# Kernel tuning notes

Measured on AMD Instinct MI355X. Metric: run time of the kernel, lower is better.

## Reference

```python
import jax, jax.numpy as jnp
import numpy as np

N = 20000   # nodes
E = 320000  # edges
F0 = 32     # num_features
H = 8       # GAT heads
G = 64      # graphs in batch


def setup_inputs() -> dict:
    key = jax.random.key(0)
    ks = jax.random.split(key, 16)
    def p(k, shape, s=0.05):
        return jax.random.normal(k, shape, jnp.float32) * s
    d = {}
    d['x'] = jax.random.normal(ks[0], (N, F0), jnp.float32)
    d['edge_index'] = jax.random.randint(ks[1], (2, E), 0, N, dtype=jnp.int32)
    d['edge_weights'] = jax.random.uniform(ks[2], (E,), jnp.float32)
    d['batch'] = jnp.sort(jax.random.randint(ks[3], (N,), 0, G, dtype=jnp.int32))
    # GATConv(32 -> 32, heads=8)
    d['W_gat'] = p(ks[4], (F0, H * F0)); d['att_src'] = p(ks[5], (H, F0))
    d['att_dst'] = p(ks[6], (H, F0));    d['b_gat'] = jnp.zeros((H * F0,), jnp.float32)
    # residual Linear(256 -> 1024) (widened so the residual add is shape-consistent)
    d['W_res'] = p(ks[7], (H * F0, 1024)); d['b_res'] = jnp.zeros((1024,), jnp.float32)
    # GCNConv(256 -> 512) + BN1
    d['W2'] = p(ks[8], (H * F0, 512)); d['b2'] = jnp.zeros((512,), jnp.float32)
    d['g1'] = jnp.ones((512,), jnp.float32); d['be1'] = jnp.zeros((512,), jnp.float32)
    d['m1'] = jnp.zeros((512,), jnp.float32); d['v1'] = jnp.ones((512,), jnp.float32)
    # GCNConv(512 -> 1024) + BN2
    d['W3'] = p(ks[9], (512, 1024)); d['b3'] = jnp.zeros((1024,), jnp.float32)
    d['g2'] = jnp.ones((1024,), jnp.float32); d['be2'] = jnp.zeros((1024,), jnp.float32)
    d['m2'] = jnp.zeros((1024,), jnp.float32); d['v2'] = jnp.ones((1024,), jnp.float32)
    # head
    d['Wf1'] = p(ks[10], (1024, 256)); d['bf1'] = jnp.zeros((256,), jnp.float32)
    d['Wf2'] = p(ks[11], (256, 2));    d['bf2'] = jnp.zeros((2,), jnp.float32)
    return d


def _add_self_loops(edge_index, edge_weight, n):
    loop = jnp.arange(n, dtype=edge_index.dtype)
    ei = jnp.concatenate([edge_index, jnp.stack([loop, loop])], axis=1)
    ew = jnp.concatenate([edge_weight, jnp.ones((n,), edge_weight.dtype)])
    return ei, ew


def _gat(x, edge_index, W, att_src, att_dst, b, n):
    # PyG GATConv, concat=True, eval (attention dropout off). Self-loops already added.
    src, dst = edge_index[0], edge_index[1]
    h = (x @ W).reshape(n, H, -1)                    # [N,H,C]
    a_s = jnp.einsum('nhc,hc->nh', h, att_src)        # [N,H]
    a_d = jnp.einsum('nhc,hc->nh', h, att_dst)
    e = jax.nn.leaky_relu(a_s[src] + a_d[dst], 0.2)   # [E,H]
    m = jax.ops.segment_max(e, dst, num_segments=n)   # softmax over incoming edges
    ex = jnp.exp(e - m[dst])
    s = jax.ops.segment_sum(ex, dst, num_segments=n)
    alpha = ex / s[dst]
    out = jax.ops.segment_sum(h[src] * alpha[:, :, None], dst, num_segments=n)
    return out.reshape(n, -1) + b                     # [N,H*C]


def _gcn(x, edge_index, w, W, b, n):
    # PyG GCNConv with symmetric normalization; self-loops (weight 1) already added.
    src, dst = edge_index[0], edge_index[1]
    deg = jax.ops.segment_sum(w, dst, num_segments=n)
    dinv = jnp.where(deg > 0, jax.lax.rsqrt(jnp.maximum(deg, 1e-12)), 0.0)
    norm = dinv[src] * w * dinv[dst]                  # [E]
    h = x @ W                                         # transform first (cheaper)
    return jax.ops.segment_sum(h[src] * norm[:, None], dst, num_segments=n) + b


def _bn(x, g, b, m, v):
    return g * (x - m) * jax.lax.rsqrt(v + 1e-5) + b


def reference(x, edge_index, edge_weights, batch, W_gat, att_src, att_dst, b_gat,
              W_res, b_res, W2, b2, g1, be1, m1, v1, W3, b3, g2, be2, m2, v2,
              Wf1, bf1, Wf2, bf2):
    n = x.shape[0]
    ei, ew = _add_self_loops(edge_index, edge_weights, n)
    h = jax.nn.relu(_gat(x, ei, W_gat, att_src, att_dst, b_gat, n))   # [N,256]
    res = h @ W_res + b_res                                           # [N,1024]
    h = _gcn(h, ei, ew, W2, b2, n)                                    # [N,512]
    h = jax.nn.relu(_bn(h, g1, be1, m1, v1))
    h = _gcn(h, ei, ew, W3, b3, n)                                    # [N,1024]
    h = jax.nn.relu(_bn(h, g2, be2, m2, v2))
    h = h + res
    pooled = jax.ops.segment_max(h, batch, num_segments=G)            # global max pool [G,1024]
    z = jax.nn.relu(pooled @ Wf1 + bf1)                               # dropout is eval no-op
    return z @ Wf2 + bf2                                              # [G,2]
```

## Files before the change

kernel.cpp:

```cpp
#include <hip/hip_runtime.h>
#include <hip/hip_bf16.h>

#define NN 20000
#define EE 320000
#define GG 64
#define EN (EE + NN)
#define MT 157
#define SB 79

typedef float f32x4 __attribute__((ext_vector_type(4)));
typedef __bf16 bf16x4 __attribute__((ext_vector_type(4)));
typedef __bf16 bf16x8 __attribute__((ext_vector_type(8)));

__device__ __forceinline__ void gl_lds16(const void* g, void* l) {
    __builtin_amdgcn_global_load_lds((const __attribute__((address_space(1))) void*)g,
                                     (__attribute__((address_space(3))) void*)l, 16, 0, 0);
}

__global__ void sentinel_kernel(float* out, int n) {
    int i = blockIdx.x * 256 + threadIdx.x;
    if (i < n) out[i] = 12345.0f;
}

__global__ void init_kernel(int* deg_cnt, float* deg_w, int* fill, float* pooled) {
    int i = blockIdx.x * 256 + threadIdx.x;
    if (i < NN) { deg_cnt[i] = 1; deg_w[i] = 1.0f; fill[i] = 0; }
    if (i < GG * 1024) pooled[i] = -INFINITY;
}

__global__ void deg_kernel(const int* __restrict__ ei, const float* __restrict__ ew,
                           int* deg_cnt, float* deg_w) {
    int e = blockIdx.x * 256 + threadIdx.x;
    if (e >= EE) return;
    int dst = ei[EE + e];
    atomicAdd(&deg_cnt[dst], 1);
    atomicAdd(&deg_w[dst], ew[e]);
}

__global__ __launch_bounds__(256) void scan_blocks(const int* __restrict__ deg_cnt, int* __restrict__ bsum) {
    __shared__ int red[256];
    int tid = threadIdx.x, i = blockIdx.x * 256 + tid;
    red[tid] = (i < NN) ? deg_cnt[i] : 0;
    __syncthreads();
    for (int s = 128; s > 0; s >>= 1) { if (tid < s) red[tid] += red[tid + s]; __syncthreads(); }
    if (tid == 0) bsum[blockIdx.x] = red[0];
}

__global__ void scan_top(int* __restrict__ bsum, int* __restrict__ rowptr) {
    if (threadIdx.x == 0) {
        int run = 0;
        for (int i = 0; i < SB; i++) { int t = bsum[i]; bsum[i] = run; run += t; }
        rowptr[NN] = run;
    }
}

__global__ __launch_bounds__(256) void scan_write(const int* __restrict__ deg_cnt,
                                                  const int* __restrict__ bsum, int* __restrict__ rowptr) {
    __shared__ int sc[256];
    int tid = threadIdx.x, b = blockIdx.x, i = b * 256 + tid;
    int v = (i < NN) ? deg_cnt[i] : 0;
    sc[tid] = v;
    __syncthreads();
    for (int ofs = 1; ofs < 256; ofs <<= 1) {
        int t = (tid >= ofs) ? sc[tid - ofs] : 0;
        __syncthreads();
        sc[tid] += t;
        __syncthreads();
    }
    if (i < NN) rowptr[i] = bsum[b] + sc[tid] - v;
}

__global__ void fill_kernel(const int* __restrict__ ei, const float* __restrict__ ew,
                            const float* __restrict__ deg_w, const int* __restrict__ rowptr,
                            int* fill, int* __restrict__ csr_src, float* __restrict__ csr_norm) {
    int e = blockIdx.x * 256 + threadIdx.x;
    if (e >= EN) return;
    int src, dst; float w;
    if (e < EE) { src = ei[e]; dst = ei[EE + e]; w = ew[e]; }
    else        { src = dst = e - EE; w = 1.0f; }
    int pos = atomicAdd(&fill[dst], 1);
    int slot = rowptr[dst] + pos;
    csr_src[slot] = src;
    csr_norm[slot] = rsqrtf(deg_w[src]) * w * rsqrtf(deg_w[dst]);
}

__global__ __launch_bounds__(256) void convert_all(
    const float* __restrict__ W2, const float* __restrict__ W3, const float* __restrict__ Wres,
    __bf16* __restrict__ W2t, __bf16* __restrict__ W3t, __bf16* __restrict__ Wrt)
{
    __shared__ float tile[64][65];
    int b = blockIdx.x;
    const float* W; __bf16* Wt; int K, N, bx, by;
    if (b < 32)       { W = W2;   Wt = W2t; K = 256; N = 512;  int bb = b;       bx = bb & 7;  by = bb >> 3; }
    else if (b < 160) { W = W3;   Wt = W3t; K = 512; N = 1024; int bb = b - 32;  bx = bb & 15; by = bb >> 4; }
    else              { W = Wres; Wt = Wrt; K = 256; N = 1024; int bb = b - 160; bx = bb & 15; by = bb >> 4; }
    int kb = by * 64, nb = bx * 64;
    int tx = threadIdx.x & 63, ty = threadIdx.x >> 6;
#pragma unroll
    for (int i = ty; i < 64; i += 4)
        tile[i][tx] = W[(size_t)(kb + i) * N + nb + tx];
    __syncthreads();
#pragma unroll
    for (int i = ty; i < 64; i += 4)
        Wt[(size_t)(nb + i) * K + kb + tx] = (__bf16)tile[tx][i];
}


__global__ __launch_bounds__(256) void a_compute(
    const float* __restrict__ x, const float* __restrict__ W,
    const float* __restrict__ att_s, const float* __restrict__ att_d,
    float* __restrict__ a_s, float* __restrict__ a_d)
{
    __shared__ float wss[8][32], wsd[8][32];
    __shared__ float xs[32][33];
    int tid = threadIdx.x;
    {
        int h = tid >> 5, k = tid & 31;
        float s = 0.f, d = 0.f;
#pragma unroll
        for (int c = 0; c < 32; c++) {
            float wv = W[k * 256 + h * 32 + c];
            s += wv * att_s[h * 32 + c];
            d += wv * att_d[h * 32 + c];
        }
        wss[h][k] = s; wsd[h][k] = d;
    }
    __syncthreads();
    for (int n0 = blockIdx.x * 32; n0 < NN; n0 += gridDim.x * 32) {
#pragma unroll
        for (int i = 0; i < 4; i++) {
            int idx = tid + i * 256;
            xs[idx >> 5][idx & 31] = x[(size_t)n0 * 32 + idx];
        }
        __syncthreads();
        int nl = tid >> 3, h = tid & 7;
        float s = 0.f, d = 0.f;
#pragma unroll
        for (int k = 0; k < 32; k++) {
            float xv = xs[nl][k];
            s += xv * wss[h][k];
            d += xv * wsd[h][k];
        }
        a_s[(n0 + nl) * 8 + h] = s;
        a_d[(n0 + nl) * 8 + h] = d;
        __syncthreads();
    }
}

__global__ __launch_bounds__(256) void gat_agg_x(
    const int* __restrict__ rowptr, const int* __restrict__ csr_src,
    const float* __restrict__ a_s, const float* __restrict__ a_d,
    const float* __restrict__ x, __bf16* __restrict__ xagg)
{
    int widx = threadIdx.x >> 6, lane = threadIdx.x & 63;
    int node = blockIdx.x * 4 + widx;
    int base = rowptr[node], deg = rowptr[node + 1] - base;
    int hA = lane & 7, eslot = lane >> 3;
    int c = lane & 31, half = lane >> 5;
    float adA = a_d[node * 8 + hA];
    float acc0[4] = {}, acc1[4] = {};

    if (deg <= 64) {
        int sv = (lane < deg) ? csr_src[base + lane] : 0;
        float ev[8];
        float psum = 0.f;
#pragma unroll
        for (int j = 0; j < 8; j++) {
            int e = j * 8 + eslot;
            float v = 0.f;
            if (e < deg) {
                int src = __shfl(sv, e);
                float t = a_s[src * 8 + hA] + adA;
                t = (t > 0.f) ? t : 0.2f * t;
                v = __expf(t);
            }
            ev[j] = v;
            psum += v;
        }
#pragma unroll
        for (int m = 8; m <= 32; m <<= 1) psum += __shfl_xor(psum, m);
        float sinv[4];
#pragma unroll
        for (int jj = 0; jj < 4; jj++) sinv[jj] = 1.f / __shfl(psum, half * 4 + jj);
#pragma unroll
        for (int j = 0; j < 8; j++) {
            if (j * 8 >= deg) break;
            int lim = min(8, deg - j * 8);
            int t = 0;
            for (; t + 1 < lim; t += 2) {
                int srcA = __shfl(sv, j * 8 + t), srcB = __shfl(sv, j * 8 + t + 1);
                float xvA = x[(size_t)srcA * 32 + c];
                float xvB = x[(size_t)srcB * 32 + c];
#pragma unroll
                for (int jj = 0; jj < 4; jj++) {
                    float aA = __shfl(ev[j], (t << 3) | (half * 4 + jj)) * sinv[jj];
                    float aB = __shfl(ev[j], ((t + 1) << 3) | (half * 4 + jj)) * sinv[jj];
                    acc0[jj] += aA * xvA;
                    acc1[jj] += aB * xvB;
                }
            }
            if (t < lim) {
                int src = __shfl(sv, j * 8 + t);
                float xv = x[(size_t)src * 32 + c];
#pragma unroll
                for (int jj = 0; jj < 4; jj++) {
                    float a = __shfl(ev[j], (t << 3) | (half * 4 + jj)) * sinv[jj];
                    acc0[jj] += a * xv;
                }
            }
        }
    } else {
        float sum = 0.f;
        for (int e = 0; e < deg; e++) {
            int src = csr_src[base + e];
            float t = a_s[src * 8 + hA] + adA;
            t = (t > 0.f) ? t : 0.2f * t;
            sum += __expf(t);
        }
        float sinv[4], ad4[4];
#pragma unroll
        for (int jj = 0; jj < 4; jj++) {
            sinv[jj] = 1.f / __shfl(sum, half * 4 + jj);
            ad4[jj] = a_d[node * 8 + half * 4 + jj];
        }
        for (int e = 0; e < deg; e++) {
            int src = csr_src[base + e];
            float xv = x[(size_t)src * 32 + c];
#pragma unroll
            for (int jj = 0; jj < 4; jj++) {
                float t = a_s[src * 8 + half * 4 + jj] + ad4[jj];
                t = (t > 0.f) ? t : 0.2f * t;
                acc0[jj] += __expf(t) * sinv[jj] * xv;
            }
        }
    }
#pragma unroll
    for (int jj = 0; jj < 4; jj++)
        xagg[(size_t)node * 256 + (half * 4 + jj) * 32 + c] = (__bf16)(acc0[jj] + acc1[jj]);
}

__global__ __launch_bounds__(256) void gat_post(
    const __bf16* __restrict__ xagg, const float* __restrict__ W,
    const float* __restrict__ b_gat, __bf16* __restrict__ h1)
{
    __shared__ float Ws[32 * 256];
    int tid = threadIdx.x;
#pragma unroll
    for (int k = 0; k < 32; k++) Ws[k * 256 + tid] = W[k * 256 + tid];
    float bg = b_gat[tid];
    int lbase = tid & 32;
    __syncthreads();
    for (int n = blockIdx.x; n < NN; n += gridDim.x) {
        float xv = (float)xagg[(size_t)n * 256 + tid];
        float acc = 0.f;
#pragma unroll
        for (int k = 0; k < 32; k++) acc += __shfl(xv, lbase + k) * Ws[k * 256 + tid];
        h1[(size_t)n * 256 + tid] = (__bf16)fmaxf(acc + bg, 0.f);
    }
}

template <int C, int SPLIT>
__global__ __launch_bounds__(256) void gcn_agg(
    const int* __restrict__ rowptr, const int* __restrict__ csr_src,
    const float* __restrict__ csr_norm, const __bf16* __restrict__ feat,
    __bf16* __restrict__ out)
{
    constexpr int V = C / (64 * SPLIT);
    int widx = threadIdx.x >> 6, lane = threadIdx.x & 63;
    int node = blockIdx.x * (4 / SPLIT) + widx / SPLIT;
    int half = widx % SPLIT;
    int coff = half * (C / SPLIT) + lane * V;
    int base = rowptr[node], deg = rowptr[node + 1] - base;
    float acc0[V], acc1[V], acc2[V], acc3[V];
#pragma unroll
    for (int j = 0; j < V; j++) { acc0[j] = 0.f; acc1[j] = 0.f; acc2[j] = 0.f; acc3[j] = 0.f; }
    const __bf16* fb = feat + coff;
    typedef __bf16 bf16v __attribute__((ext_vector_type(V)));
    for (int e0 = 0; e0 < deg; e0 += 64) {
        int cnt = min(64, deg - e0);
        int sv = 0; float wv = 0.f;
        if (lane < cnt) { sv = csr_src[base + e0 + lane]; wv = csr_norm[base + e0 + lane]; }
        int s = 0;
        for (; s + 3 < cnt; s += 4) {
            int sA = __shfl(sv, s),     sB = __shfl(sv, s + 1);
            int sC = __shfl(sv, s + 2), sD = __shfl(sv, s + 3);
            float wA = __shfl(wv, s),     wB = __shfl(wv, s + 1);
            float wC = __shfl(wv, s + 2), wD = __shfl(wv, s + 3);
            bf16v fA = *(const bf16v*)(fb + (size_t)sA * C);
            bf16v fB = *(const bf16v*)(fb + (size_t)sB * C);
            bf16v fC = *(const bf16v*)(fb + (size_t)sC * C);
            bf16v fD = *(const bf16v*)(fb + (size_t)sD * C);
#pragma unroll
            for (int j = 0; j < V; j++) {
                acc0[j] += wA * (float)fA[j]; acc1[j] += wB * (float)fB[j];
                acc2[j] += wC * (float)fC[j]; acc3[j] += wD * (float)fD[j];
            }
        }
        for (; s < cnt; s++) {
            int src = __shfl(sv, s);
            float w = __shfl(wv, s);
            bf16v f = *(const bf16v*)(fb + (size_t)src * C);
#pragma unroll
            for (int j = 0; j < V; j++) acc0[j] += w * (float)f[j];
        }
    }
    bf16v o;
#pragma unroll
    for (int j = 0; j < V; j++) o[j] = (__bf16)((acc0[j] + acc1[j]) + (acc2[j] + acc3[j]));
    *(bf16v*)(out + (size_t)node * C + coff) = o;
}


__device__ __forceinline__ void stage_async64(
    const __bf16* __restrict__ A, int K, const __bf16* __restrict__ Wt,
    int bm, int bn, int k0, int tid, __bf16* As, __bf16* Bs)
{
#pragma unroll
    for (int i = 0; i < 4; i++) {
        int j = i * 256 + tid;
        int r = j >> 3, c = j & 7;
        const __bf16* gp = A + (size_t)(bm + r) * K + k0 + ((c ^ (r & 7)) * 8);
        gl_lds16(gp, As + (size_t)(j & ~63) * 8);
    }
#pragma unroll
    for (int i = 0; i < 4; i++) {
        int j = i * 256 + tid;
        int r = j >> 3, c = j & 7;
        const __bf16* gp = Wt + (size_t)(bn + r) * K + k0 + ((c ^ (r & 7)) * 8);
        gl_lds16(gp, Bs + (size_t)(j & ~63) * 8);
    }
}

__device__ __forceinline__ void mfma_step64(
    const __bf16* As, const __bf16* Bs, int wr, int wc, int l16, int q, f32x4 (&acc)[4][4])
{
#pragma unroll
    for (int ks = 0; ks < 2; ks++) {
        bf16x8 af[4], bfv[4];
#pragma unroll
        for (int mt = 0; mt < 4; mt++) {
            int row = wr * 64 + mt * 16 + l16;
            af[mt] = *(const bf16x8*)(As + row * 64 + (((ks * 4 + q) ^ (row & 7)) * 8));
        }
#pragma unroll
        for (int nt = 0; nt < 4; nt++) {
            int row = wc * 64 + nt * 16 + l16;
            bfv[nt] = *(const bf16x8*)(Bs + row * 64 + (((ks * 4 + q) ^ (row & 7)) * 8));
        }
#pragma unroll
        for (int mt = 0; mt < 4; mt++)
#pragma unroll
            for (int nt = 0; nt < 4; nt++)
                acc[mt][nt] = __builtin_amdgcn_mfma_f32_16x16x32_bf16(af[mt], bfv[nt], acc[mt][nt], 0, 0, 0);
    }
}

__device__ __forceinline__ void gemm_loop(
    const __bf16* __restrict__ A, int K, const __bf16* __restrict__ Wt,
    int bm, int bn, int tid, int wr, int wc, int l16, int q,
    __bf16* As, __bf16* Bs, f32x4 (&acc)[4][4])
{
    for (int k0 = 0; k0 < K; k0 += 64) {
        stage_async64(A, K, Wt, bm, bn, k0, tid, As, Bs);
        __syncthreads();
        mfma_step64(As, Bs, wr, wc, l16, q, acc);
        __syncthreads();
    }
}

__global__ __launch_bounds__(256) void gemm_bn_relu(
    const __bf16* __restrict__ A, const __bf16* __restrict__ Wt,
    int M, int K, int Nc,
    const float* __restrict__ bias,
    const float* __restrict__ g, const float* __restrict__ be,
    const float* __restrict__ mu, const float* __restrict__ var,
    __bf16* __restrict__ C)
{
    __shared__ __bf16 As[128 * 64];
    __shared__ __bf16 Bs[128 * 64];
    int tid = threadIdx.x;
    int w = tid >> 6, wr = w >> 1, wc = w & 1;
    int l = tid & 63, q = l >> 4, l16 = l & 15;
    int i = blockIdx.x;
    int k = (i & 3) * MT + (i >> 2);
    int bm = (k >> 2) * 128, bn = (k & 3) * 128;
    f32x4 acc[4][4] = {};
    gemm_loop(A, K, Wt, bm, bn, tid, wr, wc, l16, q, As, Bs, acc);
#pragma unroll
    for (int nt = 0; nt < 4; nt++) {
        int gn = bn + wc * 64 + nt * 16 + l16;
        float s = g[gn] * rsqrtf(var[gn] + 1e-5f);
        float t = be[gn] - mu[gn] * s;
        float bv = bias[gn];
#pragma unroll
        for (int mt = 0; mt < 4; mt++)
#pragma unroll
            for (int r = 0; r < 4; r++) {
                int gm = bm + wr * 64 + mt * 16 + q * 4 + r;
                if (gm < M) C[(size_t)gm * Nc + gn] = (__bf16)fmaxf((acc[mt][nt][r] + bv) * s + t, 0.f);
            }
    }
}

__device__ __forceinline__ void atomicMaxFloat(float* addr, float value) {
    if (value >= 0.f) atomicMax((int*)addr, __float_as_int(value));
    else              atomicMin((unsigned int*)addr, __float_as_uint(value));
}

__global__ __launch_bounds__(256) void gemm_final(
    const __bf16* __restrict__ A1, const __bf16* __restrict__ W3t,
    const __bf16* __restrict__ A2, const __bf16* __restrict__ Wrt,
    const float* __restrict__ b3, const float* __restrict__ bres,
    const float* __restrict__ g, const float* __restrict__ be,
    const float* __restrict__ mu, const float* __restrict__ var,
    const int* __restrict__ batch, float* __restrict__ pooled)
{
    const int M = NN;
    __shared__ __bf16 As[128 * 64];
    __shared__ __bf16 Bs[128 * 64];
    __shared__ int bat[128];
    int tid = threadIdx.x;
    int w = tid >> 6, wr = w >> 1, wc = w & 1;
    int l = tid & 63, q = l >> 4, l16 = l & 15;
    int i = blockIdx.x;
    int k = (i & 7) * MT + (i >> 3);
    int bm = (k >> 3) * 128, bn = (k & 7) * 128;
    if (tid < 128) bat[tid] = (bm + tid < M) ? batch[bm + tid] : -1;
    f32x4 acc[4][4] = {};
    f32x4 accR[4][4] = {};
    gemm_loop(A1, 512, W3t, bm, bn, tid, wr, wc, l16, q, As, Bs, acc);
    gemm_loop(A2, 256, Wrt, bm, bn, tid, wr, wc, l16, q, As, Bs, accR);
#pragma unroll
    for (int nt = 0; nt < 4; nt++) {
        int gn = bn + wc * 64 + nt * 16 + l16;
        float s = g[gn] * rsqrtf(var[gn] + 1e-5f);
        float t = be[gn] - mu[gn] * s;
        float bv3 = b3[gn];
        float bvr = bres[gn];
        int cb = -1; float run = 0.f;
#pragma unroll
        for (int mt = 0; mt < 4; mt++)
#pragma unroll
            for (int r = 0; r < 4; r++) {
                int lr = wr * 64 + mt * 16 + q * 4 + r;
                int id = bat[lr];
                if (id < 0) continue;
                float v = fmaxf((acc[mt][nt][r] + bv3) * s + t, 0.f) + accR[mt][nt][r] + bvr;
                if (id == cb) run = fmaxf(run, v);
                else {
                    if (cb >= 0) atomicMaxFloat(&pooled[cb * 1024 + gn], run);
                    cb = id; run = v;
                }
            }
        if (cb >= 0) atomicMaxFloat(&pooled[cb * 1024 + gn], run);
    }
}

__global__ __launch_bounds__(256) void head_kernel(
    const float* __restrict__ pooled, const float* __restrict__ Wf1, const float* __restrict__ bf1,
    const float* __restrict__ Wf2, const float* __restrict__ bf2, float* __restrict__ out)
{
    int gph = blockIdx.x, tid = threadIdx.x;
    __shared__ float prow[1024];
    __shared__ float zred[256];
    for (int i = tid; i < 1024; i += 256) prow[i] = pooled[gph * 1024 + i];
    __syncthreads();
    float z = 0.f;
    for (int k = 0; k < 1024; k++) z += prow[k] * Wf1[k * 256 + tid];
    z = fmaxf(z + bf1[tid], 0.f);
    for (int c = 0; c < 2; c++) {
        zred[tid] = z * Wf2[tid * 2 + c];
        __syncthreads();
        for (int s = 128; s > 0; s >>= 1) { if (tid < s) zred[tid] += zred[tid + s]; __syncthreads(); }
        if (tid == 0) out[gph * 2 + c] = zred[0] + bf2[c];
        __syncthreads();
    }
}

extern "C" void kernel_launch(void* const* d_in, const int* in_sizes, int n_in,
                              void* d_out, int out_size, void* d_ws, size_t ws_size,
                              hipStream_t stream) {
    const float* x       = (const float*)d_in[0];
    const int*   ei      = (const int*)d_in[1];
    const float* ew      = (const float*)d_in[2];
    const int*   batch   = (const int*)d_in[3];
    const float* W_gat   = (const float*)d_in[4];
    const float* att_src = (const float*)d_in[5];
    const float* att_dst = (const float*)d_in[6];
    const float* b_gat   = (const float*)d_in[7];
    const float* W_res   = (const float*)d_in[8];
    const float* b_res   = (const float*)d_in[9];
    const float* W2      = (const float*)d_in[10];
    const float* b2v     = (const float*)d_in[11];
    const float* g1      = (const float*)d_in[12];
    const float* be1     = (const float*)d_in[13];
    const float* m1      = (const float*)d_in[14];
    const float* v1      = (const float*)d_in[15];
    const float* W3      = (const float*)d_in[16];
    const float* b3      = (const float*)d_in[17];
    const float* g2      = (const float*)d_in[18];
    const float* be2     = (const float*)d_in[19];
    const float* m2      = (const float*)d_in[20];
    const float* v2      = (const float*)d_in[21];
    const float* Wf1     = (const float*)d_in[22];
    const float* bf1     = (const float*)d_in[23];
    const float* Wf2     = (const float*)d_in[24];
    const float* bf2v    = (const float*)d_in[25];
    float* out           = (float*)d_out;

    char* ws = (char*)d_ws;
    size_t off = 0;
    auto alloc = [&](size_t bytes) { size_t o = off; off += (bytes + 255) & ~(size_t)255; return o; };
    size_t o_hlin   = alloc((size_t)NN * 256 * 2);
    size_t o_h1     = alloc((size_t)NN * 256 * 2);
    size_t o_h2     = alloc((size_t)NN * 512 * 2);
    size_t o_agg2   = alloc((size_t)NN * 512 * 2);
    size_t o_as     = alloc((size_t)NN * 8 * 4);
    size_t o_ad     = alloc((size_t)NN * 8 * 4);
    size_t o_degc   = alloc((size_t)NN * 4);
    size_t o_degw   = alloc((size_t)NN * 4);
    size_t o_rowptr = alloc((size_t)(NN + 1) * 4);
    size_t o_fill   = alloc((size_t)NN * 4);
    size_t o_bsum   = alloc((size_t)SB * 4);
    size_t o_csrs   = alloc((size_t)EN * 4);
    size_t o_csrn   = alloc((size_t)EN * 4);
    size_t o_pool   = alloc((size_t)GG * 1024 * 4);
    size_t o_w2t    = alloc((size_t)512 * 256 * 2);
    size_t o_w3t    = alloc((size_t)1024 * 512 * 2);
    size_t o_wrt    = alloc((size_t)1024 * 256 * 2);
    if (off > ws_size) {
        sentinel_kernel<<<(out_size + 255) / 256, 256, 0, stream>>>(out, out_size);
        return;
    }

    __bf16* xagg   = (__bf16*)(ws + o_hlin);
    __bf16* agg1   = xagg;
    __bf16* h1     = (__bf16*)(ws + o_h1);
    __bf16* h2     = (__bf16*)(ws + o_h2);
    __bf16* agg2   = (__bf16*)(ws + o_agg2);
    float*  a_s    = (float*)(ws + o_as);
    float*  a_d    = (float*)(ws + o_ad);
    int*    degc   = (int*)(ws + o_degc);
    float*  degw   = (float*)(ws + o_degw);
    int*    rowptr = (int*)(ws + o_rowptr);
    int*    fillb  = (int*)(ws + o_fill);
    int*    bsum   = (int*)(ws + o_bsum);
    int*    csrs   = (int*)(ws + o_csrs);
    float*  csrn   = (float*)(ws + o_csrn);
    float*  pooled = (float*)(ws + o_pool);
    __bf16* W2t    = (__bf16*)(ws + o_w2t);
    __bf16* W3t    = (__bf16*)(ws + o_w3t);
    __bf16* Wrt    = (__bf16*)(ws + o_wrt);

    convert_all<<<224, 256, 0, stream>>>(W2, W3, W_res, W2t, W3t, Wrt);
    a_compute<<<128, 256, 0, stream>>>(x, W_gat, att_src, att_dst, a_s, a_d);

    init_kernel<<<256, 256, 0, stream>>>(degc, degw, fillb, pooled);
    deg_kernel<<<(EE + 255) / 256, 256, 0, stream>>>(ei, ew, degc, degw);
    scan_blocks<<<SB, 256, 0, stream>>>(degc, bsum);
    scan_top<<<1, 64, 0, stream>>>(bsum, rowptr);
    scan_write<<<SB, 256, 0, stream>>>(degc, bsum, rowptr);
    fill_kernel<<<(EN + 255) / 256, 256, 0, stream>>>(ei, ew, degw, rowptr, fillb, csrs, csrn);

    gat_agg_x<<<NN / 4, 256, 0, stream>>>(rowptr, csrs, a_s, a_d, x, xagg);
    gat_post<<<1280, 256, 0, stream>>>(xagg, W_gat, b_gat, h1);

    gcn_agg<256, 1><<<NN / 4, 256, 0, stream>>>(rowptr, csrs, csrn, h1, agg1);
    gemm_bn_relu<<<4 * MT, 256, 0, stream>>>(agg1, W2t, NN, 256, 512, b2v,
        g1, be1, m1, v1, h2);
    gcn_agg<512, 2><<<NN / 2, 256, 0, stream>>>(rowptr, csrs, csrn, h2, agg2);
    gemm_final<<<8 * MT, 256, 0, stream>>>(agg2, W3t, h1, Wrt,
        b3, b_res, g2, be2, m2, v2, batch, pooled);

    head_kernel<<<GG, 256, 0, stream>>>(pooled, Wf1, bf1, Wf2, bf2v, out);
}
```

Before: 421.6 us.

## Pack CSR src/norm into int2, fold scan_top into scan_write, unroll GAT gather

Stores each CSR entry as a packed int2 (source index plus norm bits) so the GCN aggregation reads one 8-byte load per edge instead of two separate arrays. Removes the single-thread scan_top launch: each scan_write block now reduces the preceding block sums itself and the last block writes rowptr[NN]. Unrolls the GAT feature gather from 2 to 4 edges per iteration with extra accumulators to expose more memory-level parallelism. The GAT kernel now loads 8-byte entries when it only needs the index, and each scan block does a small redundant reduction.

```diff
diff --git a/kernel.cpp b/kernel.cpp
--- a/kernel.cpp
+++ b/kernel.cpp
@@ -46,18 +46,16 @@
     if (tid == 0) bsum[blockIdx.x] = red[0];
 }
 
-__global__ void scan_top(int* __restrict__ bsum, int* __restrict__ rowptr) {
-    if (threadIdx.x == 0) {
-        int run = 0;
-        for (int i = 0; i < SB; i++) { int t = bsum[i]; bsum[i] = run; run += t; }
-        rowptr[NN] = run;
-    }
-}
-
 __global__ __launch_bounds__(256) void scan_write(const int* __restrict__ deg_cnt,
                                                   const int* __restrict__ bsum, int* __restrict__ rowptr) {
     __shared__ int sc[256];
+    __shared__ int red[256];
     int tid = threadIdx.x, b = blockIdx.x, i = b * 256 + tid;
+    red[tid] = (tid < b && tid < SB) ? bsum[tid] : 0;
+    __syncthreads();
+    for (int s = 128; s > 0; s >>= 1) { if (tid < s) red[tid] += red[tid + s]; __syncthreads(); }
+    int boff = red[0];
+    __syncthreads();
     int v = (i < NN) ? deg_cnt[i] : 0;
     sc[tid] = v;
     __syncthreads();
@@ -67,12 +65,13 @@
         sc[tid] += t;
         __syncthreads();
     }
-    if (i < NN) rowptr[i] = bsum[b] + sc[tid] - v;
+    if (i < NN) rowptr[i] = boff + sc[tid] - v;
+    if (b == SB - 1 && tid == 255) rowptr[NN] = boff + sc[255];
 }
 
 __global__ void fill_kernel(const int* __restrict__ ei, const float* __restrict__ ew,
                             const float* __restrict__ deg_w, const int* __restrict__ rowptr,
-                            int* fill, int* __restrict__ csr_src, float* __restrict__ csr_norm) {
+                            int* fill, int2* __restrict__ csre) {
     int e = blockIdx.x * 256 + threadIdx.x;
     if (e >= EN) return;
     int src, dst; float w;
@@ -80,8 +79,8 @@
     else        { src = dst = e - EE; w = 1.0f; }
     int pos = atomicAdd(&fill[dst], 1);
     int slot = rowptr[dst] + pos;
-    csr_src[slot] = src;
-    csr_norm[slot] = rsqrtf(deg_w[src]) * w * rsqrtf(deg_w[dst]);
+    float norm = rsqrtf(deg_w[src]) * w * rsqrtf(deg_w[dst]);
+    csre[slot] = make_int2(src, __float_as_int(norm));
 }
 
 __global__ __launch_bounds__(256) void convert_all(
@@ -148,7 +147,7 @@
 }
 
 __global__ __launch_bounds__(256) void gat_agg_x(
-    const int* __restrict__ rowptr, const int* __restrict__ csr_src,
+    const int* __restrict__ rowptr, const int2* __restrict__ csre,
     const float* __restrict__ a_s, const float* __restrict__ a_d,
     const float* __restrict__ x, __bf16* __restrict__ xagg)
 {
@@ -158,10 +157,10 @@
     int hA = lane & 7, eslot = lane >> 3;
     int c = lane & 31, half = lane >> 5;
     float adA = a_d[node * 8 + hA];
-    float acc0[4] = {}, acc1[4] = {};
+    float acc0[4] = {}, acc1[4] = {}, acc2[4] = {}, acc3[4] = {};
 
     if (deg <= 64) {
-        int sv = (lane < deg) ? csr_src[base + lane] : 0;
+        int sv = (lane < deg) ? csre[base + lane].x : 0;
         float ev[8];
         float psum = 0.f;
 #pragma unroll
@@ -187,19 +186,23 @@
             if (j * 8 >= deg) break;
             int lim = min(8, deg - j * 8);
             int t = 0;
-            for (; t + 1 < lim; t += 2) {
-                int srcA = __shfl(sv, j * 8 + t), srcB = __shfl(sv, j * 8 + t + 1);
-                float xvA = x[(size_t)srcA * 32 + c];
-                float xvB = x[(size_t)srcB * 32 + c];
+            for (; t + 3 < lim; t += 4) {
+                int sA = __shfl(sv, j * 8 + t),     sB = __shfl(sv, j * 8 + t + 1);
+                int sC = __shfl(sv, j * 8 + t + 2), sD = __shfl(sv, j * 8 + t + 3);
+                float xvA = x[(size_t)sA * 32 + c];
+                float xvB = x[(size_t)sB * 32 + c];
+                float xvC = x[(size_t)sC * 32 + c];
+                float xvD = x[(size_t)sD * 32 + c];
 #pragma unroll
                 for (int jj = 0; jj < 4; jj++) {
-                    float aA = __shfl(ev[j], (t << 3) | (half * 4 + jj)) * sinv[jj];
-                    float aB = __shfl(ev[j], ((t + 1) << 3) | (half * 4 + jj)) * sinv[jj];
-                    acc0[jj] += aA * xvA;
-                    acc1[jj] += aB * xvB;
+                    int hb = half * 4 + jj;
+                    acc0[jj] += __shfl(ev[j], (t << 3) | hb) * sinv[jj] * xvA;
+                    acc1[jj] += __shfl(ev[j], ((t + 1) << 3) | hb) * sinv[jj] * xvB;
+                    acc2[jj] += __shfl(ev[j], ((t + 2) << 3) | hb) * sinv[jj] * xvC;
+                    acc3[jj] += __shfl(ev[j], ((t + 3) << 3) | hb) * sinv[jj] * xvD;
                 }
             }
-            if (t < lim) {
+            for (; t < lim; t++) {
                 int src = __shfl(sv, j * 8 + t);
                 float xv = x[(size_t)src * 32 + c];
 #pragma unroll
@@ -212,7 +215,7 @@
     } else {
         float sum = 0.f;
         for (int e = 0; e < deg; e++) {
-            int src = csr_src[base + e];
+            int src = csre[base + e].x;
             float t = a_s[src * 8 + hA] + adA;
             t = (t > 0.f) ? t : 0.2f * t;
             sum += __expf(t);
@@ -224,7 +227,7 @@
             ad4[jj] = a_d[node * 8 + half * 4 + jj];
         }
         for (int e = 0; e < deg; e++) {
-            int src = csr_src[base + e];
+            int src = csre[base + e].x;
             float xv = x[(size_t)src * 32 + c];
 #pragma unroll
             for (int jj = 0; jj < 4; jj++) {
@@ -236,7 +239,8 @@
     }
 #pragma unroll
     for (int jj = 0; jj < 4; jj++)
-        xagg[(size_t)node * 256 + (half * 4 + jj) * 32 + c] = (__bf16)(acc0[jj] + acc1[jj]);
+        xagg[(size_t)node * 256 + (half * 4 + jj) * 32 + c] =
+            (__bf16)((acc0[jj] + acc1[jj]) + (acc2[jj] + acc3[jj]));
 }
 
 __global__ __launch_bounds__(256) void gat_post(
@@ -261,9 +265,8 @@
 
 template <int C, int SPLIT>
 __global__ __launch_bounds__(256) void gcn_agg(
-    const int* __restrict__ rowptr, const int* __restrict__ csr_src,
-    const float* __restrict__ csr_norm, const __bf16* __restrict__ feat,
-    __bf16* __restrict__ out)
+    const int* __restrict__ rowptr, const int2* __restrict__ csre,
+    const __bf16* __restrict__ feat, __bf16* __restrict__ out)
 {
     constexpr int V = C / (64 * SPLIT);
     int widx = threadIdx.x >> 6, lane = threadIdx.x & 63;
@@ -279,7 +282,7 @@
     for (int e0 = 0; e0 < deg; e0 += 64) {
         int cnt = min(64, deg - e0);
         int sv = 0; float wv = 0.f;
-        if (lane < cnt) { sv = csr_src[base + e0 + lane]; wv = csr_norm[base + e0 + lane]; }
+        if (lane < cnt) { int2 m = csre[base + e0 + lane]; sv = m.x; wv = __int_as_float(m.y); }
         int s = 0;
         for (; s + 3 < cnt; s += 4) {
             int sA = __shfl(sv, s),     sB = __shfl(sv, s + 1);
@@ -522,8 +525,7 @@
     size_t o_rowptr = alloc((size_t)(NN + 1) * 4);
     size_t o_fill   = alloc((size_t)NN * 4);
     size_t o_bsum   = alloc((size_t)SB * 4);
-    size_t o_csrs   = alloc((size_t)EN * 4);
-    size_t o_csrn   = alloc((size_t)EN * 4);
+    size_t o_csre   = alloc((size_t)EN * 8);
     size_t o_pool   = alloc((size_t)GG * 1024 * 4);
     size_t o_w2t    = alloc((size_t)512 * 256 * 2);
     size_t o_w3t    = alloc((size_t)1024 * 512 * 2);
@@ -545,8 +547,7 @@
     int*    rowptr = (int*)(ws + o_rowptr);
     int*    fillb  = (int*)(ws + o_fill);
     int*    bsum   = (int*)(ws + o_bsum);
-    int*    csrs   = (int*)(ws + o_csrs);
-    float*  csrn   = (float*)(ws + o_csrn);
+    int2*   csre   = (int2*)(ws + o_csre);
     float*  pooled = (float*)(ws + o_pool);
     __bf16* W2t    = (__bf16*)(ws + o_w2t);
     __bf16* W3t    = (__bf16*)(ws + o_w3t);
@@ -558,17 +559,16 @@
     init_kernel<<<256, 256, 0, stream>>>(degc, degw, fillb, pooled);
     deg_kernel<<<(EE + 255) / 256, 256, 0, stream>>>(ei, ew, degc, degw);
     scan_blocks<<<SB, 256, 0, stream>>>(degc, bsum);
-    scan_top<<<1, 64, 0, stream>>>(bsum, rowptr);
     scan_write<<<SB, 256, 0, stream>>>(degc, bsum, rowptr);
-    fill_kernel<<<(EN + 255) / 256, 256, 0, stream>>>(ei, ew, degw, rowptr, fillb, csrs, csrn);
-
-    gat_agg_x<<<NN / 4, 256, 0, stream>>>(rowptr, csrs, a_s, a_d, x, xagg);
+    fill_kernel<<<(EN + 255) / 256, 256, 0, stream>>>(ei, ew, degw, rowptr, fillb, csre);
+
+    gat_agg_x<<<NN / 4, 256, 0, stream>>>(rowptr, csre, a_s, a_d, x, xagg);
     gat_post<<<1280, 256, 0, stream>>>(xagg, W_gat, b_gat, h1);
 
-    gcn_agg<256, 1><<<NN / 4, 256, 0, stream>>>(rowptr, csrs, csrn, h1, agg1);
+    gcn_agg<256, 1><<<NN / 4, 256, 0, stream>>>(rowptr, csre, h1, agg1);
     gemm_bn_relu<<<4 * MT, 256, 0, stream>>>(agg1, W2t, NN, 256, 512, b2v,
         g1, be1, m1, v1, h2);
-    gcn_agg<512, 2><<<NN / 2, 256, 0, stream>>>(rowptr, csrs, csrn, h2, agg2);
+    gcn_agg<512, 2><<<NN / 2, 256, 0, stream>>>(rowptr, csre, h2, agg2);
     gemm_final<<<8 * MT, 256, 0, stream>>>(agg2, W3t, h1, Wrt,
         b3, b_res, g2, be2, m2, v2, batch, pooled);
 
```

After: 419.0 us. Within noise of the previous version (-0.6%).
